# Performance work log

Measured on AMD Instinct MI355X. Metric: run time of the kernel, lower is better.

Reference implementation:

```python
import jax, jax.numpy as jnp
import numpy as np

ROWS = 256
COLS = 256
EPS = 1e-8


def _radius_bins(rows, cols):
    # Same construction as SpectralLoss.__init__: integer radius per rfft bin,
    # ifftshifted along the row axis to match torch.rfft layout.
    shift_rows = rows // 2
    cols_onesided = cols // 2 + 1
    idx = np.indices((rows, cols_onesided)) - np.array([[[shift_rows]], [[0]]])
    r = np.sqrt(idx[0] ** 2 + idx[1] ** 2).astype(int)
    r = np.fft.ifftshift(r, axes=0)
    return r  # [rows, cols_onesided], values in [0, r_max]


def setup_inputs() -> dict:
    key = jax.random.key(0)
    k1, k2 = jax.random.split(key)
    r = _radius_bins(ROWS, COLS)
    vector_length = int(r.max()) + 1  # 182
    data = jax.random.normal(k1, (128, 3, ROWS, COLS), dtype=jnp.float32)
    mean = jax.random.uniform(k2, (vector_length,), dtype=jnp.float32)
    radius = jnp.asarray(r, dtype=jnp.int32)
    return {"data": data, "mean": mean, "radius": radius}


def reference(data, mean, radius):
    L = mean.shape[0]  # vector_length = r_max + 1
    # RGB -> luma (as in SpectralLoss.fft)
    gray = 0.299 * data[:, 0] + 0.587 * data[:, 1] + 0.114 * data[:, 2]  # [B,H,W]
    f = jnp.fft.rfft2(gray)  # [B, H, W//2+1]
    power = f.real ** 2 + f.imag ** 2  # sum of squared re/im parts
    fft_abs = 20.0 * jnp.log(power + EPS)  # [B, H, Wc]
    # Radial histogram: segment-mean keyed on integer radius (replaces the
    # original dense one-hot mask broadcast of shape [B, L, H, Wc]).
    seg = radius.reshape(-1)  # [N] with N = H*Wc
    B = fft_abs.shape[0]
    flat = fft_abs.reshape(B, -1).T  # [N, B]
    sums = jax.ops.segment_sum(flat, seg, num_segments=L)  # [L, B]
    counts = jax.ops.segment_sum(jnp.ones_like(flat[:, :1]), seg, num_segments=L)  # [L, 1]
    profile = (sums / counts).T  # [B, L]
    # Per-sample min-max normalization (same order of ops as torch code)
    profile = profile - jnp.min(profile, axis=1, keepdims=True)
    profile = profile / jnp.max(profile, axis=1, keepdims=True)
    # L1 loss with reduction='sum' against the target mean profile
    return jnp.sum(jnp.abs(profile - mean[None, :]))
```

## Files before the change

kernel.cpp:

```cpp
#include <hip/hip_runtime.h>
#include <cmath>

#define B_   128
#define H_   256
#define W_   256
#define WC_  129
#define L_   182
#define NG_  33
#define PI_F 3.14159265358979f

__device__ __forceinline__ void fft256_wave(float vr[4], float vi[4], int l) {
  float c0, s0;
  __sincosf(-2.f * PI_F * (float)l / 256.f, &s0, &c0);
  {
    float ur = vr[0] + vr[2], ui = vi[0] + vi[2];
    float dr = vr[0] - vr[2], di = vi[0] - vi[2];
    vr[0] = ur; vi[0] = ui;
    vr[2] = dr * c0 - di * s0; vi[2] = dr * s0 + di * c0;
    float c1 = s0, s1 = -c0;
    ur = vr[1] + vr[3]; ui = vi[1] + vi[3];
    dr = vr[1] - vr[3]; di = vi[1] - vi[3];
    vr[1] = ur; vi[1] = ui;
    vr[3] = dr * c1 - di * s1; vi[3] = dr * s1 + di * c1;
  }
  {
    float c2 = c0 * c0 - s0 * s0, s2 = 2.f * c0 * s0;
    float ur = vr[0] + vr[1], ui = vi[0] + vi[1];
    float dr = vr[0] - vr[1], di = vi[0] - vi[1];
    vr[0] = ur; vi[0] = ui;
    vr[1] = dr * c2 - di * s2; vi[1] = dr * s2 + di * c2;
    ur = vr[2] + vr[3]; ui = vi[2] + vi[3];
    dr = vr[2] - vr[3]; di = vi[2] - vi[3];
    vr[2] = ur; vi[2] = ui;
    vr[3] = dr * c2 - di * s2; vi[3] = dr * s2 + di * c2;
  }
  #pragma unroll
  for (int h = 32; h >= 1; h >>= 1) {
    int i = l & (h - 1);
    float c, s;
    __sincosf(-PI_F * (float)i / (float)h, &s, &c);
    bool up = (l & h) != 0;
    float cc = up ? c : 1.f;
    float ss = up ? s : 0.f;
    float sgn = up ? -1.f : 1.f;
    #pragma unroll
    for (int j = 0; j < 4; ++j) {
      float br = __shfl_xor(vr[j], h, 64);
      float bi = __shfl_xor(vi[j], h, 64);
      float tr = fmaf(sgn, vr[j], br);
      float ti = fmaf(sgn, vi[j], bi);
      vr[j] = tr * cc - ti * ss;
      vi[j] = tr * ss + ti * cc;
    }
  }
}

#define P1_PAIRS 16
#define P1_STRIDE 259

__global__ __launch_bounds__(1024) void pass1_kernel(
    const float* __restrict__ data, float4* __restrict__ inter4) {
  __shared__ float2 tile[P1_PAIRS * P1_STRIDE];
  int tid = threadIdx.x;
  int w = tid >> 6, l = tid & 63;
  int b = blockIdx.x >> 3;
  int row0 = (blockIdx.x & 7) * 32;
  int rowA = row0 + 2 * w;
  const float* pA = data + ((size_t)b * 3) * (H_ * W_) + (size_t)rowA * W_;
  float vr[4], vi[4];
  #pragma unroll
  for (int j = 0; j < 4; ++j) {
    int i = l + 64 * j;
    float r = pA[i], g = pA[H_ * W_ + i], bl = pA[2 * H_ * W_ + i];
    vr[j] = fmaf(0.299f, r, fmaf(0.587f, g, 0.114f * bl));
    r = pA[W_ + i]; g = pA[H_ * W_ + W_ + i]; bl = pA[2 * H_ * W_ + W_ + i];
    vi[j] = fmaf(0.299f, r, fmaf(0.587f, g, 0.114f * bl));
  }
  fft256_wave(vr, vi, l);
  #pragma unroll
  for (int j = 0; j < 4; ++j)
    tile[w * P1_STRIDE + l + 64 * j] = make_float2(vr[j], vi[j]);
  __syncthreads();
  for (int f = tid; f < WC_ * P1_PAIRS; f += 1024) {
    int k = f >> 4;
    int p = f & 15;
    int qk  = (int)(__brev((unsigned)k) >> 24);
    int qnk = (int)(__brev((unsigned)((256 - k) & 255)) >> 24);
    float2 Zk  = tile[p * P1_STRIDE + qk];
    float2 Znk = tile[p * P1_STRIDE + qnk];
    float4 o;
    o.x = 0.5f * (Zk.x + Znk.x);
    o.y = 0.5f * (Zk.y - Znk.y);
    o.z = 0.5f * (Zk.y + Znk.y);
    o.w = 0.5f * (Znk.x - Zk.x);
    inter4[((((size_t)b * WC_ + k) * H_ + row0) >> 1) + p] = o;
  }
}

__global__ __launch_bounds__(256) void pass2_kernel(
    const float2* __restrict__ inter, const int* __restrict__ radius,
    float* __restrict__ partial, float* __restrict__ cntpart) {
  __shared__ float lbins[L_];
  __shared__ float lcnt[L_];
  int tid = threadIdx.x;
  int wv = tid >> 6, l = tid & 63;
  int b = blockIdx.x / NG_;
  int g = blockIdx.x - b * NG_;
  int k = g * 4 + wv;
  bool do_cnt = (b == 0);
  for (int i = tid; i < L_; i += 256) lbins[i] = 0.f;
  if (do_cnt)
    for (int i = tid; i < L_; i += 256) lcnt[i] = 0.f;
  __syncthreads();
  if (k < WC_) {
    const float2* p = inter + ((size_t)b * WC_ + k) * H_;
    float vr[4], vi[4];
    #pragma unroll
    for (int j = 0; j < 4; ++j) {
      float2 v = p[l + 64 * j];
      vr[j] = v.x; vi[j] = v.y;
    }
    fft256_wave(vr, vi, l);
    int rb = 4 * (int)(__brev((unsigned)l) >> 26);
    #pragma unroll
    for (int j = 0; j < 4; ++j) {
      int rf = rb + ((j == 1) ? 2 : (j == 2) ? 1 : j);
      int bin = radius[rf * WC_ + k];
      float pw = vr[j] * vr[j] + vi[j] * vi[j];
      float val = 20.f * __logf(pw + 1e-8f);
      atomicAdd(&lbins[bin], val);
      if (do_cnt) atomicAdd(&lcnt[bin], 1.f);
    }
  }
  __syncthreads();
  float* pp = partial + ((size_t)b * NG_ + g) * L_;
  for (int i = tid; i < L_; i += 256) pp[i] = lbins[i];
  if (do_cnt) {
    float* cp = cntpart + (size_t)g * L_;
    for (int i = tid; i < L_; i += 256) cp[i] = lcnt[i];
  }
}

__global__ __launch_bounds__(256) void loss_kernel(
    const float* __restrict__ partial, const float* __restrict__ cntpart,
    const float* __restrict__ mean, float* __restrict__ lpart) {
  int b = blockIdx.x;
  int t = threadIdx.x;
  __shared__ float prof[L_];
  __shared__ float red[256];
  float acc = 0.f, csum = 0.f;
  if (t < L_) {
    const float* pb = partial + (size_t)b * NG_ * L_;
    #pragma unroll 3
    for (int g = 0; g < NG_; ++g) {
      acc  += pb[g * L_ + t];
      csum += cntpart[g * L_ + t];
    }
    prof[t] = acc / csum;
  }
  __syncthreads();
  red[t] = (t < L_) ? prof[t] : INFINITY;
  __syncthreads();
  for (int s = 128; s > 0; s >>= 1) {
    if (t < s) red[t] = fminf(red[t], red[t + s]);
    __syncthreads();
  }
  float mn = red[0];
  __syncthreads();
  red[t] = (t < L_) ? (prof[t] - mn) : -INFINITY;
  __syncthreads();
  for (int s = 128; s > 0; s >>= 1) {
    if (t < s) red[t] = fmaxf(red[t], red[t + s]);
    __syncthreads();
  }
  float mx = red[0];
  __syncthreads();
  red[t] = (t < L_) ? fabsf((prof[t] - mn) / mx - mean[t]) : 0.f;
  __syncthreads();
  for (int s = 128; s > 0; s >>= 1) {
    if (t < s) red[t] += red[t + s];
    __syncthreads();
  }
  if (t == 0) lpart[b] = red[0];
}

__global__ __launch_bounds__(64) void final_kernel(
    const float* __restrict__ lpart, float* __restrict__ out) {
  int l = threadIdx.x;
  float v = lpart[l] + lpart[l + 64];
  #pragma unroll
  for (int h = 32; h >= 1; h >>= 1) v += __shfl_xor(v, h, 64);
  if (l == 0) out[0] = v;
}

extern "C" void kernel_launch(void* const* d_in, const int* in_sizes, int n_in,
                              void* d_out, int out_size, void* d_ws, size_t ws_size,
                              hipStream_t stream) {
  const float* data   = (const float*)d_in[0];
  const float* mean   = (const float*)d_in[1];
  const int*   radius = (const int*)d_in[2];
  float* out = (float*)d_out;

  float2* inter = (float2*)d_ws;
  size_t inter_bytes = (size_t)B_ * WC_ * H_ * sizeof(float2);
  float* partial = (float*)((char*)d_ws + inter_bytes);
  float* cntpart = partial + (size_t)B_ * NG_ * L_;
  float* lpart   = cntpart + (size_t)NG_ * L_;

  pass1_kernel<<<B_ * 8, 1024, 0, stream>>>(data, (float4*)inter);
  pass2_kernel<<<B_ * NG_, 256, 0, stream>>>(inter, radius, partial, cntpart);
  loss_kernel<<<B_, 256, 0, stream>>>(partial, cntpart, mean, lpart);
  final_kernel<<<1, 64, 0, stream>>>(lpart, out);
}
```

Before: 194.3 us.

## Fuse radial binning with per-sample loss and compute bin counts in pass1

Each batch sample's column FFTs, radial binning and min-max normalized L1 loss now run in one 1024-thread block, removing the separate loss kernel and the partial-sum buffer. Bin counts are computed once by an extra block appended to pass1. This removes a launch and intermediate global traffic, but pass2 now launches only 128 blocks that loop sequentially over columns, which reduces parallelism and may leave many compute units idle.

```diff
diff --git a/kernel.cpp b/kernel.cpp
--- a/kernel.cpp
+++ b/kernel.cpp
@@ -6,7 +6,6 @@
 #define W_   256
 #define WC_  129
 #define L_   182
-#define NG_  33
 #define PI_F 3.14159265358979f
 
 __device__ __forceinline__ void fft256_wave(float vr[4], float vi[4], int l) {
@@ -59,9 +58,20 @@
 #define P1_STRIDE 259
 
 __global__ __launch_bounds__(1024) void pass1_kernel(
-    const float* __restrict__ data, float4* __restrict__ inter4) {
+    const float* __restrict__ data, float4* __restrict__ inter4,
+    const int* __restrict__ radius, float* __restrict__ cnt) {
   __shared__ float2 tile[P1_PAIRS * P1_STRIDE];
   int tid = threadIdx.x;
+  if (blockIdx.x == B_ * 8) {
+    float* lcnt = (float*)tile;
+    for (int i = tid; i < L_; i += 1024) lcnt[i] = 0.f;
+    __syncthreads();
+    for (int i = tid; i < H_ * WC_; i += 1024)
+      atomicAdd(&lcnt[radius[i]], 1.f);
+    __syncthreads();
+    for (int i = tid; i < L_; i += 1024) cnt[i] = lcnt[i];
+    return;
+  }
   int w = tid >> 6, l = tid & 63;
   int b = blockIdx.x >> 3;
   int row0 = (blockIdx.x & 7) * 32;
@@ -97,91 +107,61 @@
   }
 }
 
-__global__ __launch_bounds__(256) void pass2_kernel(
+__global__ __launch_bounds__(1024) void pass2_fused(
     const float2* __restrict__ inter, const int* __restrict__ radius,
-    float* __restrict__ partial, float* __restrict__ cntpart) {
+    const float* __restrict__ cnt, const float* __restrict__ mean,
+    float* __restrict__ lpart) {
   __shared__ float lbins[L_];
-  __shared__ float lcnt[L_];
   int tid = threadIdx.x;
   int wv = tid >> 6, l = tid & 63;
-  int b = blockIdx.x / NG_;
-  int g = blockIdx.x - b * NG_;
-  int k = g * 4 + wv;
-  bool do_cnt = (b == 0);
-  for (int i = tid; i < L_; i += 256) lbins[i] = 0.f;
-  if (do_cnt)
-    for (int i = tid; i < L_; i += 256) lcnt[i] = 0.f;
+  int b = blockIdx.x;
+  for (int i = tid; i < L_; i += 1024) lbins[i] = 0.f;
   __syncthreads();
-  if (k < WC_) {
-    const float2* p = inter + ((size_t)b * WC_ + k) * H_;
-    float vr[4], vi[4];
-    #pragma unroll
-    for (int j = 0; j < 4; ++j) {
-      float2 v = p[l + 64 * j];
-      vr[j] = v.x; vi[j] = v.y;
-    }
-    fft256_wave(vr, vi, l);
-    int rb = 4 * (int)(__brev((unsigned)l) >> 26);
-    #pragma unroll
-    for (int j = 0; j < 4; ++j) {
-      int rf = rb + ((j == 1) ? 2 : (j == 2) ? 1 : j);
-      int bin = radius[rf * WC_ + k];
-      float pw = vr[j] * vr[j] + vi[j] * vi[j];
-      float val = 20.f * __logf(pw + 1e-8f);
-      atomicAdd(&lbins[bin], val);
-      if (do_cnt) atomicAdd(&lcnt[bin], 1.f);
+  #pragma unroll 1
+  for (int round = 0; round < 9; ++round) {
+    int k = round * 16 + wv;
+    if (k < WC_) {
+      const float2* p = inter + ((size_t)b * WC_ + k) * H_;
+      float vr[4], vi[4];
+      #pragma unroll
+      for (int j = 0; j < 4; ++j) {
+        float2 v = p[l + 64 * j];
+        vr[j] = v.x; vi[j] = v.y;
+      }
+      fft256_wave(vr, vi, l);
+      int rb = 4 * (int)(__brev((unsigned)l) >> 26);
+      #pragma unroll
+      for (int j = 0; j < 4; ++j) {
+        int rf = rb + ((j == 1) ? 2 : (j == 2) ? 1 : j);
+        int bin = radius[rf * WC_ + k];
+        float pw = vr[j] * vr[j] + vi[j] * vi[j];
+        float val = 20.f * __logf(pw + 1e-8f);
+        atomicAdd(&lbins[bin], val);
+      }
     }
   }
   __syncthreads();
-  float* pp = partial + ((size_t)b * NG_ + g) * L_;
-  for (int i = tid; i < L_; i += 256) pp[i] = lbins[i];
-  if (do_cnt) {
-    float* cp = cntpart + (size_t)g * L_;
-    for (int i = tid; i < L_; i += 256) cp[i] = lcnt[i];
+  if (wv == 0) {
+    float pa = lbins[l] / cnt[l];
+    float pb = lbins[l + 64] / cnt[l + 64];
+    bool v2 = (l + 128) < L_;
+    float pc = v2 ? lbins[l + 128] / cnt[l + 128] : 0.f;
+    float mn = fminf(pa, pb);
+    if (v2) mn = fminf(mn, pc);
+    #pragma unroll
+    for (int h = 32; h >= 1; h >>= 1) mn = fminf(mn, __shfl_xor(mn, h, 64));
+    float mxr = fmaxf(pa, pb);
+    if (v2) mxr = fmaxf(mxr, pc);
+    #pragma unroll
+    for (int h = 32; h >= 1; h >>= 1) mxr = fmaxf(mxr, __shfl_xor(mxr, h, 64));
+    float mx = mxr - mn;
+    float s = fabsf((pa - mn) / mx - mean[l]) +
+              fabsf((pb - mn) / mx - mean[l + 64]);
+    if (v2) s += fabsf((pc - mn) / mx - mean[l + 128]);
+    #pragma unroll
+    for (int h = 32; h >= 1; h >>= 1) s += __shfl_xor(s, h, 64);
+    if (l == 0) lpart[b] = s;
   }
-}
-
-__global__ __launch_bounds__(256) void loss_kernel(
-    const float* __restrict__ partial, const float* __restrict__ cntpart,
-    const float* __restrict__ mean, float* __restrict__ lpart) {
-  int b = blockIdx.x;
-  int t = threadIdx.x;
-  __shared__ float prof[L_];
-  __shared__ float red[256];
-  float acc = 0.f, csum = 0.f;
-  if (t < L_) {
-    const float* pb = partial + (size_t)b * NG_ * L_;
-    #pragma unroll 3
-    for (int g = 0; g < NG_; ++g) {
-      acc  += pb[g * L_ + t];
-      csum += cntpart[g * L_ + t];
-    }
-    prof[t] = acc / csum;
-  }
-  __syncthreads();
-  red[t] = (t < L_) ? prof[t] : INFINITY;
-  __syncthreads();
-  for (int s = 128; s > 0; s >>= 1) {
-    if (t < s) red[t] = fminf(red[t], red[t + s]);
-    __syncthreads();
-  }
-  float mn = red[0];
-  __syncthreads();
-  red[t] = (t < L_) ? (prof[t] - mn) : -INFINITY;
-  __syncthreads();
-  for (int s = 128; s > 0; s >>= 1) {
-    if (t < s) red[t] = fmaxf(red[t], red[t + s]);
-    __syncthreads();
-  }
-  float mx = red[0];
-  __syncthreads();
-  red[t] = (t < L_) ? fabsf((prof[t] - mn) / mx - mean[t]) : 0.f;
-  __syncthreads();
-  for (int s = 128; s > 0; s >>= 1) {
-    if (t < s) red[t] += red[t + s];
-    __syncthreads();
-  }
-  if (t == 0) lpart[b] = red[0];
 }
 
 __global__ __launch_bounds__(64) void final_kernel(
@@ -203,12 +183,10 @@
 
   float2* inter = (float2*)d_ws;
   size_t inter_bytes = (size_t)B_ * WC_ * H_ * sizeof(float2);
-  float* partial = (float*)((char*)d_ws + inter_bytes);
-  float* cntpart = partial + (size_t)B_ * NG_ * L_;
-  float* lpart   = cntpart + (size_t)NG_ * L_;
+  float* cnt   = (float*)((char*)d_ws + inter_bytes);
+  float* lpart = cnt + 256;
 
-  pass1_kernel<<<B_ * 8, 1024, 0, stream>>>(data, (float4*)inter);
-  pass2_kernel<<<B_ * NG_, 256, 0, stream>>>(inter, radius, partial, cntpart);
-  loss_kernel<<<B_, 256, 0, stream>>>(partial, cntpart, mean, lpart);
+  pass1_kernel<<<B_ * 8 + 1, 1024, 0, stream>>>(data, (float4*)inter, radius, cnt);
+  pass2_fused<<<B_, 1024, 0, stream>>>(inter, radius, cnt, mean, lpart);
   final_kernel<<<1, 64, 0, stream>>>(lpart, out);
 }
```

New measurement: 259.3 us. 1.33x slower.

## Process two FFTs per wavefront and use single-wave loss reduction

Applied to the files above, without the earlier changes.

The wave-level FFT now handles two 256-point transforms per wavefront (8 values per lane), sharing twiddle computation and raising instruction-level parallelism. Pass1 switches to 256-thread blocks that each process 16 rows, and pass2 processes 8 columns per block, which halves the partial-histogram count. The loss kernel is rewritten as a single 64-lane wave that uses shuffle reductions instead of shared-memory tree reductions with barriers. Register pressure per lane rises, which may lower occupancy.

```diff
diff --git a/kernel.cpp b/kernel.cpp
--- a/kernel.cpp
+++ b/kernel.cpp
@@ -6,33 +6,32 @@
 #define W_   256
 #define WC_  129
 #define L_   182
-#define NG_  33
+#define NG_  17
 #define PI_F 3.14159265358979f
 
-__device__ __forceinline__ void fft256_wave(float vr[4], float vi[4], int l) {
+__device__ __forceinline__ void fft256x2_wave(float vr[8], float vi[8], int l) {
   float c0, s0;
   __sincosf(-2.f * PI_F * (float)l / 256.f, &s0, &c0);
-  {
-    float ur = vr[0] + vr[2], ui = vi[0] + vi[2];
-    float dr = vr[0] - vr[2], di = vi[0] - vi[2];
-    vr[0] = ur; vi[0] = ui;
-    vr[2] = dr * c0 - di * s0; vi[2] = dr * s0 + di * c0;
-    float c1 = s0, s1 = -c0;
-    ur = vr[1] + vr[3]; ui = vi[1] + vi[3];
-    dr = vr[1] - vr[3]; di = vi[1] - vi[3];
-    vr[1] = ur; vi[1] = ui;
-    vr[3] = dr * c1 - di * s1; vi[3] = dr * s1 + di * c1;
-  }
-  {
-    float c2 = c0 * c0 - s0 * s0, s2 = 2.f * c0 * s0;
-    float ur = vr[0] + vr[1], ui = vi[0] + vi[1];
-    float dr = vr[0] - vr[1], di = vi[0] - vi[1];
-    vr[0] = ur; vi[0] = ui;
-    vr[1] = dr * c2 - di * s2; vi[1] = dr * s2 + di * c2;
-    ur = vr[2] + vr[3]; ui = vi[2] + vi[3];
-    dr = vr[2] - vr[3]; di = vi[2] - vi[3];
-    vr[2] = ur; vi[2] = ui;
-    vr[3] = dr * c2 - di * s2; vi[3] = dr * s2 + di * c2;
+  float c1 = s0, s1 = -c0;
+  float c2 = c0 * c0 - s0 * s0, s2 = 2.f * c0 * s0;
+  #pragma unroll
+  for (int f = 0; f < 8; f += 4) {
+    float ur = vr[f+0] + vr[f+2], ui = vi[f+0] + vi[f+2];
+    float dr = vr[f+0] - vr[f+2], di = vi[f+0] - vi[f+2];
+    vr[f+0] = ur; vi[f+0] = ui;
+    vr[f+2] = dr * c0 - di * s0; vi[f+2] = dr * s0 + di * c0;
+    ur = vr[f+1] + vr[f+3]; ui = vi[f+1] + vi[f+3];
+    dr = vr[f+1] - vr[f+3]; di = vi[f+1] - vi[f+3];
+    vr[f+1] = ur; vi[f+1] = ui;
+    vr[f+3] = dr * c1 - di * s1; vi[f+3] = dr * s1 + di * c1;
+    ur = vr[f+0] + vr[f+1]; ui = vi[f+0] + vi[f+1];
+    dr = vr[f+0] - vr[f+1]; di = vi[f+0] - vi[f+1];
+    vr[f+0] = ur; vi[f+0] = ui;
+    vr[f+1] = dr * c2 - di * s2; vi[f+1] = dr * s2 + di * c2;
+    ur = vr[f+2] + vr[f+3]; ui = vi[f+2] + vi[f+3];
+    dr = vr[f+2] - vr[f+3]; di = vi[f+2] - vi[f+3];
+    vr[f+2] = ur; vi[f+2] = ui;
+    vr[f+3] = dr * c2 - di * s2; vi[f+3] = dr * s2 + di * c2;
   }
   #pragma unroll
   for (int h = 32; h >= 1; h >>= 1) {
@@ -44,7 +43,7 @@
     float ss = up ? s : 0.f;
     float sgn = up ? -1.f : 1.f;
     #pragma unroll
-    for (int j = 0; j < 4; ++j) {
+    for (int j = 0; j < 8; ++j) {
       float br = __shfl_xor(vr[j], h, 64);
       float bi = __shfl_xor(vi[j], h, 64);
       float tr = fmaf(sgn, vr[j], br);
@@ -55,35 +54,41 @@
   }
 }
 
-#define P1_PAIRS 16
+#define P1_PAIRS 8
 #define P1_STRIDE 259
 
-__global__ __launch_bounds__(1024) void pass1_kernel(
+__global__ __launch_bounds__(256) void pass1_kernel(
     const float* __restrict__ data, float4* __restrict__ inter4) {
   __shared__ float2 tile[P1_PAIRS * P1_STRIDE];
   int tid = threadIdx.x;
   int w = tid >> 6, l = tid & 63;
-  int b = blockIdx.x >> 3;
-  int row0 = (blockIdx.x & 7) * 32;
-  int rowA = row0 + 2 * w;
-  const float* pA = data + ((size_t)b * 3) * (H_ * W_) + (size_t)rowA * W_;
-  float vr[4], vi[4];
+  int b = blockIdx.x >> 4;
+  int row0 = (blockIdx.x & 15) * 16;
+  const float* base = data + (size_t)b * 3 * (H_ * W_);
+  float vr[8], vi[8];
+  #pragma unroll
+  for (int f = 0; f < 2; ++f) {
+    int rowA = row0 + 2 * w + 8 * f;
+    const float* pR = base + (size_t)rowA * W_;
+    #pragma unroll
+    for (int j = 0; j < 4; ++j) {
+      int i = l + 64 * j;
+      float r = pR[i], g = pR[H_ * W_ + i], bl = pR[2 * H_ * W_ + i];
+      vr[4 * f + j] = fmaf(0.299f, r, fmaf(0.587f, g, 0.114f * bl));
+      r = pR[W_ + i]; g = pR[H_ * W_ + W_ + i]; bl = pR[2 * H_ * W_ + W_ + i];
+      vi[4 * f + j] = fmaf(0.299f, r, fmaf(0.587f, g, 0.114f * bl));
+    }
+  }
+  fft256x2_wave(vr, vi, l);
   #pragma unroll
   for (int j = 0; j < 4; ++j) {
-    int i = l + 64 * j;
-    float r = pA[i], g = pA[H_ * W_ + i], bl = pA[2 * H_ * W_ + i];
-    vr[j] = fmaf(0.299f, r, fmaf(0.587f, g, 0.114f * bl));
-    r = pA[W_ + i]; g = pA[H_ * W_ + W_ + i]; bl = pA[2 * H_ * W_ + W_ + i];
-    vi[j] = fmaf(0.299f, r, fmaf(0.587f, g, 0.114f * bl));
-  }
-  fft256_wave(vr, vi, l);
-  #pragma unroll
-  for (int j = 0; j < 4; ++j)
-    tile[w * P1_STRIDE + l + 64 * j] = make_float2(vr[j], vi[j]);
+    tile[w * P1_STRIDE + l + 64 * j]       = make_float2(vr[j],     vi[j]);
+    tile[(w + 4) * P1_STRIDE + l + 64 * j] = make_float2(vr[4 + j], vi[4 + j]);
+  }
   __syncthreads();
-  for (int f = tid; f < WC_ * P1_PAIRS; f += 1024) {
-    int k = f >> 4;
-    int p = f & 15;
+  for (int f = tid; f < WC_ * P1_PAIRS; f += 256) {
+    int k = f >> 3;
+    int p = f & 7;
     int qk  = (int)(__brev((unsigned)k) >> 24);
     int qnk = (int)(__brev((unsigned)((256 - k) & 255)) >> 24);
     float2 Zk  = tile[p * P1_STRIDE + qk];
@@ -106,29 +111,39 @@
   int wv = tid >> 6, l = tid & 63;
   int b = blockIdx.x / NG_;
   int g = blockIdx.x - b * NG_;
-  int k = g * 4 + wv;
+  int k1 = g * 8 + wv;
+  int k2 = k1 + 4;
+  bool v1 = k1 < WC_, v2 = k2 < WC_;
   bool do_cnt = (b == 0);
   for (int i = tid; i < L_; i += 256) lbins[i] = 0.f;
   if (do_cnt)
     for (int i = tid; i < L_; i += 256) lcnt[i] = 0.f;
   __syncthreads();
-  if (k < WC_) {
-    const float2* p = inter + ((size_t)b * WC_ + k) * H_;
-    float vr[4], vi[4];
-    #pragma unroll
-    for (int j = 0; j < 4; ++j) {
-      float2 v = p[l + 64 * j];
-      vr[j] = v.x; vi[j] = v.y;
-    }
-    fft256_wave(vr, vi, l);
-    int rb = 4 * (int)(__brev((unsigned)l) >> 26);
-    #pragma unroll
-    for (int j = 0; j < 4; ++j) {
-      int rf = rb + ((j == 1) ? 2 : (j == 2) ? 1 : j);
-      int bin = radius[rf * WC_ + k];
+  float vr[8], vi[8];
+  const float2* p1 = inter + ((size_t)b * WC_ + k1) * H_;
+  const float2* p2 = inter + ((size_t)b * WC_ + k2) * H_;
+  #pragma unroll
+  for (int j = 0; j < 4; ++j) {
+    float2 a = v1 ? p1[l + 64 * j] : make_float2(0.f, 0.f);
+    float2 c = v2 ? p2[l + 64 * j] : make_float2(0.f, 0.f);
+    vr[j] = a.x; vi[j] = a.y;
+    vr[4 + j] = c.x; vi[4 + j] = c.y;
+  }
+  fft256x2_wave(vr, vi, l);
+  int rb = 4 * (int)(__brev((unsigned)l) >> 26);
+  #pragma unroll
+  for (int j = 0; j < 4; ++j) {
+    int rf = rb + ((j == 1) ? 2 : (j == 2) ? 1 : j);
+    if (v1) {
+      int bin = radius[rf * WC_ + k1];
       float pw = vr[j] * vr[j] + vi[j] * vi[j];
-      float val = 20.f * __logf(pw + 1e-8f);
-      atomicAdd(&lbins[bin], val);
+      atomicAdd(&lbins[bin], 20.f * __logf(pw + 1e-8f));
+      if (do_cnt) atomicAdd(&lcnt[bin], 1.f);
+    }
+    if (v2) {
+      int bin = radius[rf * WC_ + k2];
+      float pw = vr[4 + j] * vr[4 + j] + vi[4 + j] * vi[4 + j];
+      atomicAdd(&lbins[bin], 20.f * __logf(pw + 1e-8f));
       if (do_cnt) atomicAdd(&lcnt[bin], 1.f);
     }
   }
@@ -141,47 +156,45 @@
   }
 }
 
-__global__ __launch_bounds__(256) void loss_kernel(
+__global__ __launch_bounds__(64) void loss_kernel(
     const float* __restrict__ partial, const float* __restrict__ cntpart,
     const float* __restrict__ mean, float* __restrict__ lpart) {
   int b = blockIdx.x;
-  int t = threadIdx.x;
-  __shared__ float prof[L_];
-  __shared__ float red[256];
-  float acc = 0.f, csum = 0.f;
-  if (t < L_) {
-    const float* pb = partial + (size_t)b * NG_ * L_;
-    #pragma unroll 3
+  int l = threadIdx.x;
+  const float* pb = partial + (size_t)b * NG_ * L_;
+  float s0 = 0.f, s1 = 0.f, s2 = 0.f;
+  float n0 = 0.f, n1 = 0.f, n2 = 0.f;
+  #pragma unroll 1
+  for (int g = 0; g < NG_; ++g) {
+    s0 += pb[g * L_ + l];        n0 += cntpart[g * L_ + l];
+    s1 += pb[g * L_ + l + 64];   n1 += cntpart[g * L_ + l + 64];
+  }
+  bool has2 = (l + 128) < L_;
+  if (has2) {
+    #pragma unroll 1
     for (int g = 0; g < NG_; ++g) {
-      acc  += pb[g * L_ + t];
-      csum += cntpart[g * L_ + t];
-    }
-    prof[t] = acc / csum;
-  }
-  __syncthreads();
-  red[t] = (t < L_) ? prof[t] : INFINITY;
-  __syncthreads();
-  for (int s = 128; s > 0; s >>= 1) {
-    if (t < s) red[t] = fminf(red[t], red[t + s]);
-    __syncthreads();
-  }
-  float mn = red[0];
-  __syncthreads();
-  red[t] = (t < L_) ? (prof[t] - mn) : -INFINITY;
-  __syncthreads();
-  for (int s = 128; s > 0; s >>= 1) {
-    if (t < s) red[t] = fmaxf(red[t], red[t + s]);
-    __syncthreads();
-  }
-  float mx = red[0];
-  __syncthreads();
-  red[t] = (t < L_) ? fabsf((prof[t] - mn) / mx - mean[t]) : 0.f;
-  __syncthreads();
-  for (int s = 128; s > 0; s >>= 1) {
-    if (t < s) red[t] += red[t + s];
-    __syncthreads();
-  }
-  if (t == 0) lpart[b] = red[0];
+      s2 += pb[g * L_ + l + 128];
+      n2 += cntpart[g * L_ + l + 128];
+    }
+  }
+  float pa = s0 / n0;
+  float pc = s1 / n1;
+  float pe = has2 ? (s2 / n2) : 0.f;
+  float mn = fminf(pa, pc);
+  if (has2) mn = fminf(mn, pe);
+  #pragma unroll
+  for (int h = 32; h >= 1; h >>= 1) mn = fminf(mn, __shfl_xor(mn, h, 64));
+  float mxr = fmaxf(pa, pc);
+  if (has2) mxr = fmaxf(mxr, pe);
+  #pragma unroll
+  for (int h = 32; h >= 1; h >>= 1) mxr = fmaxf(mxr, __shfl_xor(mxr, h, 64));
+  float mx = mxr - mn;
+  float s = fabsf((pa - mn) / mx - mean[l]) +
+            fabsf((pc - mn) / mx - mean[l + 64]);
+  if (has2) s += fabsf((pe - mn) / mx - mean[l + 128]);
+  #pragma unroll
+  for (int h = 32; h >= 1; h >>= 1) s += __shfl_xor(s, h, 64);
+  if (l == 0) lpart[b] = s;
 }
 
 __global__ __launch_bounds__(64) void final_kernel(
@@ -207,8 +220,8 @@
   float* cntpart = partial + (size_t)B_ * NG_ * L_;
   float* lpart   = cntpart + (size_t)NG_ * L_;
 
-  pass1_kernel<<<B_ * 8, 1024, 0, stream>>>(data, (float4*)inter);
+  pass1_kernel<<<B_ * 16, 256, 0, stream>>>(data, (float4*)inter);
   pass2_kernel<<<B_ * NG_, 256, 0, stream>>>(inter, radius, partial, cntpart);
-  loss_kernel<<<B_, 256, 0, stream>>>(partial, cntpart, mean, lpart);
+  loss_kernel<<<B_, 64, 0, stream>>>(partial, cntpart, mean, lpart);
   final_kernel<<<1, 64, 0, stream>>>(lpart, out);
 }
```

New measurement: 202.4 us. 1.04x slower.

## Stage luma in LDS with float4 loads and run two FFTs per wave

Applied to the files above, without the earlier changes.

Pass 1 now reads the RGB planes as coalesced float4 vectors, computes luma into shared memory, and then gathers row pairs from LDS. Each wave runs two interleaved 256-point FFTs through a new fft256x2_wave helper, so the twiddles are shared and there is more instruction-level parallelism. Blocks shrink from 1024 to 256 threads, and twice as many blocks cover 16 rows each. The aim is better global-load efficiency and better latency hiding in the row-FFT pass. The cost is higher register pressure from 16 live complex values per thread and extra LDS barriers.

```diff
diff --git a/kernel.cpp b/kernel.cpp
--- a/kernel.cpp
+++ b/kernel.cpp
@@ -55,35 +55,99 @@
   }
 }
 
-#define P1_PAIRS 16
+__device__ __forceinline__ void fft256x2_wave(float vr[8], float vi[8], int l) {
+  float c0, s0;
+  __sincosf(-2.f * PI_F * (float)l / 256.f, &s0, &c0);
+  float c1 = s0, s1 = -c0;
+  float c2 = c0 * c0 - s0 * s0, s2 = 2.f * c0 * s0;
+  #pragma unroll
+  for (int f = 0; f < 8; f += 4) {
+    float ur = vr[f+0] + vr[f+2], ui = vi[f+0] + vi[f+2];
+    float dr = vr[f+0] - vr[f+2], di = vi[f+0] - vi[f+2];
+    vr[f+0] = ur; vi[f+0] = ui;
+    vr[f+2] = dr * c0 - di * s0; vi[f+2] = dr * s0 + di * c0;
+    ur = vr[f+1] + vr[f+3]; ui = vi[f+1] + vi[f+3];
+    dr = vr[f+1] - vr[f+3]; di = vi[f+1] - vi[f+3];
+    vr[f+1] = ur; vi[f+1] = ui;
+    vr[f+3] = dr * c1 - di * s1; vi[f+3] = dr * s1 + di * c1;
+    ur = vr[f+0] + vr[f+1]; ui = vi[f+0] + vi[f+1];
+    dr = vr[f+0] - vr[f+1]; di = vi[f+0] - vi[f+1];
+    vr[f+0] = ur; vi[f+0] = ui;
+    vr[f+1] = dr * c2 - di * s2; vi[f+1] = dr * s2 + di * c2;
+    ur = vr[f+2] + vr[f+3]; ui = vi[f+2] + vi[f+3];
+    dr = vr[f+2] - vr[f+3]; di = vi[f+2] - vi[f+3];
+    vr[f+2] = ur; vi[f+2] = ui;
+    vr[f+3] = dr * c2 - di * s2; vi[f+3] = dr * s2 + di * c2;
+  }
+  #pragma unroll
+  for (int h = 32; h >= 1; h >>= 1) {
+    int i = l & (h - 1);
+    float c, s;
+    __sincosf(-PI_F * (float)i / (float)h, &s, &c);
+    bool up = (l & h) != 0;
+    float cc = up ? c : 1.f;
+    float ss = up ? s : 0.f;
+    float sgn = up ? -1.f : 1.f;
+    #pragma unroll
+    for (int j = 0; j < 8; ++j) {
+      float br = __shfl_xor(vr[j], h, 64);
+      float bi = __shfl_xor(vi[j], h, 64);
+      float tr = fmaf(sgn, vr[j], br);
+      float ti = fmaf(sgn, vi[j], bi);
+      vr[j] = tr * cc - ti * ss;
+      vi[j] = tr * ss + ti * cc;
+    }
+  }
+}
+
+#define P1_PAIRS 8
 #define P1_STRIDE 259
 
-__global__ __launch_bounds__(1024) void pass1_kernel(
+__global__ __launch_bounds__(256) void pass1_kernel(
     const float* __restrict__ data, float4* __restrict__ inter4) {
   __shared__ float2 tile[P1_PAIRS * P1_STRIDE];
+  float* luma = (float*)tile;
   int tid = threadIdx.x;
   int w = tid >> 6, l = tid & 63;
-  int b = blockIdx.x >> 3;
-  int row0 = (blockIdx.x & 7) * 32;
-  int rowA = row0 + 2 * w;
-  const float* pA = data + ((size_t)b * 3) * (H_ * W_) + (size_t)rowA * W_;
-  float vr[4], vi[4];
+  int b = blockIdx.x >> 4;
+  int row0 = (blockIdx.x & 15) * 16;
+  const float* base = data + (size_t)b * 3 * (H_ * W_) + (size_t)row0 * W_;
+  const float4* pr = (const float4*)base;
+  const float4* pg = (const float4*)(base + H_ * W_);
+  const float4* pb = (const float4*)(base + 2 * H_ * W_);
+  #pragma unroll
+  for (int it = 0; it < 4; ++it) {
+    int q = tid + 256 * it;
+    float4 r = pr[q], g = pg[q], bl = pb[q];
+    float4 o;
+    o.x = fmaf(0.299f, r.x, fmaf(0.587f, g.x, 0.114f * bl.x));
+    o.y = fmaf(0.299f, r.y, fmaf(0.587f, g.y, 0.114f * bl.y));
+    o.z = fmaf(0.299f, r.z, fmaf(0.587f, g.z, 0.114f * bl.z));
+    o.w = fmaf(0.299f, r.w, fmaf(0.587f, g.w, 0.114f * bl.w));
+    ((float4*)luma)[q] = o;
+  }
+  __syncthreads();
+  float vr[8], vi[8];
+  #pragma unroll
+  for (int f = 0; f < 2; ++f) {
+    int rA = 2 * w + 8 * f;
+    #pragma unroll
+    for (int j = 0; j < 4; ++j) {
+      vr[4 * f + j] = luma[rA * W_ + l + 64 * j];
+      vi[4 * f + j] = luma[(rA + 1) * W_ + l + 64 * j];
+    }
+  }
+  __syncthreads();
+  fft256x2_wave(vr, vi, l);
   #pragma unroll
   for (int j = 0; j < 4; ++j) {
-    int i = l + 64 * j;
-    float r = pA[i], g = pA[H_ * W_ + i], bl = pA[2 * H_ * W_ + i];
-    vr[j] = fmaf(0.299f, r, fmaf(0.587f, g, 0.114f * bl));
-    r = pA[W_ + i]; g = pA[H_ * W_ + W_ + i]; bl = pA[2 * H_ * W_ + W_ + i];
-    vi[j] = fmaf(0.299f, r, fmaf(0.587f, g, 0.114f * bl));
-  }
-  fft256_wave(vr, vi, l);
-  #pragma unroll
-  for (int j = 0; j < 4; ++j)
-    tile[w * P1_STRIDE + l + 64 * j] = make_float2(vr[j], vi[j]);
-  __syncthreads();
-  for (int f = tid; f < WC_ * P1_PAIRS; f += 1024) {
-    int k = f >> 4;
-    int p = f & 15;
+    tile[w * P1_STRIDE + l + 64 * j]       = make_float2(vr[j],     vi[j]);
+    tile[(w + 4) * P1_STRIDE + l + 64 * j] = make_float2(vr[4 + j], vi[4 + j]);
+  }
+  __syncthreads();
+  for (int f = tid; f < WC_ * P1_PAIRS; f += 256) {
+    int k = f >> 3;
+    int p = f & 7;
     int qk  = (int)(__brev((unsigned)k) >> 24);
     int qnk = (int)(__brev((unsigned)((256 - k) & 255)) >> 24);
     float2 Zk  = tile[p * P1_STRIDE + qk];
@@ -207,7 +271,7 @@
   float* cntpart = partial + (size_t)B_ * NG_ * L_;
   float* lpart   = cntpart + (size_t)NG_ * L_;
 
-  pass1_kernel<<<B_ * 8, 1024, 0, stream>>>(data, (float4*)inter);
+  pass1_kernel<<<B_ * 16, 256, 0, stream>>>(data, (float4*)inter);
   pass2_kernel<<<B_ * NG_, 256, 0, stream>>>(inter, radius, partial, cntpart);
   loss_kernel<<<B_, 256, 0, stream>>>(partial, cntpart, mean, lpart);
   final_kernel<<<1, 64, 0, stream>>>(lpart, out);
```

New measurement: 194.6 us. Within noise of the previous version (+0.1%).
